# Kernel tuning notes

Hardware: AMD Instinct MI355X
Metric: run time of the kernel (lower is better)

The kernel has to match this reference:

```python
import jax, jax.numpy as jnp
import numpy as np

B, N, D = 8, 128, 256
EPS = 1e-5


def _layernorm(x, g, b):
    m = jnp.mean(x, axis=-1, keepdims=True)
    v = jnp.mean(jnp.square(x - m), axis=-1, keepdims=True)
    return (x - m) * jax.lax.rsqrt(v + EPS) * g + b


def setup_inputs() -> dict:
    key = jax.random.key(0)
    ks = jax.random.split(key, 24)
    s = 0.05  # param init scale
    return {
        "text": jax.random.normal(ks[0], (B, N, D), jnp.float32),
        "adj1": jax.random.uniform(ks[1], (B, N, N), jnp.float32),
        "adj2": jax.random.uniform(ks[2], (B, N, N), jnp.float32),
        "edge1": jax.random.normal(ks[3], (B, N, N, D), jnp.float32) * 0.1,
        "edge2": jax.random.normal(ks[4], (B, N, N, D), jnp.float32) * 0.1,
        "textmask": jnp.ones((B, N), jnp.float32),
        "weight": jax.random.normal(ks[5], (D, D), jnp.float32) * s,
        "bias": jax.random.normal(ks[6], (D,), jnp.float32) * s,
        "gamma": jnp.ones((D,), jnp.float32),
        "beta": jnp.zeros((D,), jnp.float32),
        "fuse1_w": jax.random.normal(ks[7], (2 * D, D), jnp.float32) * s,
        "fuse2_w": jax.random.normal(ks[8], (2 * D, D), jnp.float32) * s,
        "fc3_w": jax.random.normal(ks[9], (2 * D, D), jnp.float32) * s,
        "fc1_w0": jax.random.normal(ks[10], (3 * D, D), jnp.float32) * s,
        "fc1_w1": jax.random.normal(ks[11], (D, 1), jnp.float32) * s,
        "fc1_b1": jnp.zeros((1,), jnp.float32),
        "fc2_w0": jax.random.normal(ks[12], (3 * D, D), jnp.float32) * s,
        "fc2_w1": jax.random.normal(ks[13], (D, 1), jnp.float32) * s,
        "fc2_b1": jnp.zeros((1,), jnp.float32),
        "align_lin": jax.random.normal(ks[14], (D, D), jnp.float32) * s,
        "align_bias": jax.random.normal(ks[15], (D,), jnp.float32) * s,
    }


def reference(text, adj1, adj2, edge1, edge2, textmask, weight, bias, gamma,
              beta, fuse1_w, fuse2_w, fc3_w, fc1_w0, fc1_w1, fc1_b1,
              fc2_w0, fc2_w1, fc2_b1, align_lin, align_bias):
    d = text.shape[-1]
    # ---- SelfAlignment ----
    logits = jnp.einsum('bid,bjd->bij', text @ align_lin, text)
    mask_add = (1.0 - textmask)[:, None, :] * -1e20
    probs = jax.nn.softmax(logits + mask_add, axis=-1)
    outss = jnp.einsum('bij,bjd->bid', probs, text) * textmask[..., None] + align_bias

    # ---- GCN body ----
    out = jax.nn.relu(text @ weight)  # [B,N,D]

    # edge contributions are loop-invariant: precompute once
    # torch cat([x,e]) @ W  ==  x @ W[:d] + e @ W[d:]
    e1_fuse = jnp.einsum('bijd,de->bije', edge1, fuse1_w[d:])
    e2_fuse = jnp.einsum('bijd,de->bije', edge2, fuse2_w[d:])
    e1_fc = jnp.einsum('bijd,de->bije', edge1, fc1_w0[2 * d:])
    e2_fc = jnp.einsum('bijd,de->bije', edge2, fc2_w0[2 * d:])

    denom1 = jnp.sum(adj1, axis=2, keepdims=True) + 1.0  # [B,N,1]
    denom2 = jnp.sum(adj2, axis=2, keepdims=True) + 1.0

    for _ in range(3):  # K = 3
        # text1[b,i,j] = out[b,i]; text2[b,i,j] = out[b,j]
        t_i1 = (out @ fc1_w0[:d])[:, :, None, :]        # text1 part, fc1
        t_j1 = (out @ fc1_w0[d:2 * d])[:, None, :, :]   # text2 part, fc1
        t_i2 = (out @ fc2_w0[:d])[:, :, None, :]
        t_j2 = (out @ fc2_w0[d:2 * d])[:, None, :, :]

        teout = jax.nn.relu((out @ fuse1_w[:d])[:, None, :, :] + e1_fuse)  # [B,N,N,D]
        tein = jax.nn.relu((out @ fuse2_w[:d])[:, None, :, :] + e2_fuse)

        s1 = jax.nn.sigmoid(jax.nn.relu(t_i1 + t_j1 + e1_fc) @ fc1_w1 + fc1_b1)[..., 0]  # [B,N,N]
        s2 = jax.nn.sigmoid(jax.nn.relu(t_i2 + t_j2 + e2_fc) @ fc2_w1 + fc2_b1)[..., 0]

        out1 = jnp.einsum('bij,bijd->bid', adj1 * s1, teout) / denom1
        out2 = jnp.einsum('bij,bijd->bid', adj2 * s2, tein) / denom2

        out = jax.nn.relu(out1 @ fc3_w[:d] + out2 @ fc3_w[d:]) + out + bias
        out = _layernorm(out, gamma, beta)  # dropout = identity (eval)
    return out, outss
```

## Files before the change

### kernel.cpp

```cpp
#include <hip/hip_runtime.h>

typedef unsigned short u16;
typedef unsigned int u32;
typedef __attribute__((ext_vector_type(8))) short bf16x8;
typedef __attribute__((ext_vector_type(4))) float f32x4;

__device__ __forceinline__ u16 f2bf(float f) {
  u32 u = __float_as_uint(f);
  return (u16)((u + 0x7fffu + ((u >> 16) & 1u)) >> 16);
}

__device__ __forceinline__ void glds16(const void* g, void* l) {
  __builtin_amdgcn_global_load_lds(
      (const __attribute__((address_space(1))) unsigned int*)g,
      (__attribute__((address_space(3))) unsigned int*)l, 16, 0, 0);
}

__device__ __forceinline__ float4 unpack4(const u16* p) {
  uint2 a = *(const uint2*)p;
  float4 r;
  r.x = __uint_as_float(a.x << 16);
  r.y = __uint_as_float(a.x & 0xffff0000u);
  r.z = __uint_as_float(a.y << 16);
  r.w = __uint_as_float(a.y & 0xffff0000u);
  return r;
}

__global__ __launch_bounds__(256) void gemm_edge(
    const float* __restrict__ Af, const u16* __restrict__ Bt,
    u16* __restrict__ E) {
  __shared__ __align__(16) u16 Asm[8192];
  __shared__ __align__(16) u16 Bsm[8192];
  const int tid = threadIdx.x, lane = tid & 63, w = tid >> 6;
  const int m = lane & 15, q = lane >> 4;
  const int p = blockIdx.x;
  const int rt = (p & 7) * 128 + (p >> 5);
  const int ct = (p >> 3) & 3;
  const int wrow = (w & 1) * 64, wcol = (w >> 1) * 64;
  const float* Ab = Af + (long)rt * 32768;
  const char* Bb = (const char*)Bt + (long)ct * 65536;
  f32x4 acc[4][4];
#pragma unroll
  for (int r = 0; r < 4; ++r)
#pragma unroll
    for (int c = 0; c < 4; ++c) acc[r][c] = (f32x4){0.f, 0.f, 0.f, 0.f};

  for (int kc = 0; kc < 4; ++kc) {
#pragma unroll
    for (int it = 0; it < 8; ++it) {
      int f = it * 256 + tid;
      int r = f >> 4, c4 = (f & 15) * 4;
      float4 v = *(const float4*)(Ab + (long)r * 256 + kc * 64 + c4);
      ushort4 h;
      h.x = f2bf(v.x); h.y = f2bf(v.y); h.z = f2bf(v.z); h.w = f2bf(v.w);
      *(ushort4*)((char*)Asm + r * 128 + ((c4 * 2) ^ ((r & 7) * 16))) = h;
    }
#pragma unroll
    for (int t = 0; t < 4; ++t)
      glds16(Bb + kc * 16384 + t * 4096 + tid * 16,
             (char*)Bsm + t * 4096 + tid * 16);
    __syncthreads();
#pragma unroll
    for (int s = 0; s < 2; ++s) {
      const int ko2 = (s * 32 + q * 8) * 2;
      bf16x8 av[4], bv[4];
#pragma unroll
      for (int r = 0; r < 4; ++r) {
        int row = wrow + r * 16 + m;
        av[r] = *(const bf16x8*)((const char*)Asm + row * 128 +
                                 (ko2 ^ ((row & 7) * 16)));
      }
#pragma unroll
      for (int c = 0; c < 4; ++c) {
        int col = wcol + c * 16 + m;
        bv[c] = *(const bf16x8*)((const char*)Bsm + col * 128 +
                                 (ko2 ^ ((col & 7) * 16)));
      }
#pragma unroll
      for (int r = 0; r < 4; ++r)
#pragma unroll
        for (int c = 0; c < 4; ++c)
          acc[r][c] = __builtin_amdgcn_mfma_f32_16x16x32_bf16(
              av[r], bv[c], acc[r][c], 0, 0, 0);
    }
    __syncthreads();
  }
#pragma unroll
  for (int r = 0; r < 4; ++r)
#pragma unroll
    for (int c = 0; c < 4; ++c)
#pragma unroll
      for (int g = 0; g < 4; ++g) {
        long gr = (long)rt * 128 + wrow + r * 16 + q * 4 + g;
        int gc = ct * 128 + wcol + c * 16 + m;
        E[gr * 512 + gc] = f2bf(acc[r][c][g]);
      }
}

template<int K, int RF, bool OUT_BF16, bool RELU0, bool SUM2>
__global__ __launch_bounds__(256) void gemm_mfma(
    const float* __restrict__ A, const u16* __restrict__ Bt,
    void* __restrict__ Cv, int Ntot, float* __restrict__ relu_dst,
    const float* __restrict__ A2) {
  constexpr int ROWS = RF * 16;
  constexpr int LD = 72;
  __shared__ __align__(16) u16 Asm[ROWS * LD];
  __shared__ __align__(16) u16 Bsm[256 * LD];
  const int tid = threadIdx.x;
  const int lane = tid & 63;
  const int w = tid >> 6;
  const int m = lane & 15;
  const int q = lane >> 4;
  const int wcol = w * 64;
  const long rowbase = (long)blockIdx.x * ROWS;
  const long colbase = (long)blockIdx.y * 256;
  f32x4 acc[RF][4];
#pragma unroll
  for (int r = 0; r < RF; ++r)
#pragma unroll
    for (int c = 0; c < 4; ++c) acc[r][c] = (f32x4){0.f, 0.f, 0.f, 0.f};

  for (int kc = 0; kc < K / 64; ++kc) {
    const int kb = kc * 64;
#pragma unroll
    for (int it = 0; it < RF; ++it) {
      int f = it * 256 + tid;
      int r = f >> 4, c4 = (f & 15) * 4;
      float4 v = *(const float4*)(A + (rowbase + r) * K + kb + c4);
      if (SUM2) {
        float4 v2 = *(const float4*)(A2 + (rowbase + r) * K + kb + c4);
        v.x += v2.x; v.y += v2.y; v.z += v2.z; v.w += v2.w;
      }
      ushort4 h;
      h.x = f2bf(v.x); h.y = f2bf(v.y); h.z = f2bf(v.z); h.w = f2bf(v.w);
      *(ushort4*)&Asm[r * LD + c4] = h;
    }
#pragma unroll
    for (int it = 0; it < 8; ++it) {
      int f = it * 256 + tid;
      int c = f >> 3, k8 = (f & 7) * 8;
      *(uint4*)&Bsm[c * LD + k8] =
          *(const uint4*)(Bt + (colbase + c) * K + kb + k8);
    }
    __syncthreads();
#pragma unroll
    for (int s = 0; s < 2; ++s) {
      const int ko = s * 32 + q * 8;
      bf16x8 av[RF], bv[4];
#pragma unroll
      for (int r = 0; r < RF; ++r)
        av[r] = *(const bf16x8*)&Asm[(r * 16 + m) * LD + ko];
#pragma unroll
      for (int c = 0; c < 4; ++c)
        bv[c] = *(const bf16x8*)&Bsm[(wcol + c * 16 + m) * LD + ko];
#pragma unroll
      for (int r = 0; r < RF; ++r)
#pragma unroll
        for (int c = 0; c < 4; ++c)
          acc[r][c] = __builtin_amdgcn_mfma_f32_16x16x32_bf16(
              av[r], bv[c], acc[r][c], 0, 0, 0);
    }
    __syncthreads();
  }
#pragma unroll
  for (int r = 0; r < RF; ++r)
#pragma unroll
    for (int c = 0; c < 4; ++c)
#pragma unroll
      for (int g = 0; g < 4; ++g) {
        long gr = rowbase + r * 16 + q * 4 + g;
        long gc = colbase + wcol + c * 16 + m;
        float v = acc[r][c][g];
        if (OUT_BF16) ((u16*)Cv)[gr * Ntot + gc] = f2bf(v);
        else          ((float*)Cv)[gr * Ntot + gc] = v;
        if (RELU0) {
          if (gc < 256) relu_dst[gr * 256 + gc] = fmaxf(v, 0.f);
        }
      }
}

__global__ __launch_bounds__(256) void prep_bt(
    const float* __restrict__ weight, const float* __restrict__ align_lin,
    const float* __restrict__ fuse1_w, const float* __restrict__ fuse2_w,
    const float* __restrict__ fc1_w0, const float* __restrict__ fc2_w0,
    const float* __restrict__ fc3_w,
    u16* BtE1, u16* BtE2, u16* BtW0, u16* BtLoop, u16* BtFc3) {
  int g = blockIdx.x * 256 + threadIdx.x;
  if (g < 262144) {
    int t = g & 131071;
    int col = t >> 8, k = t & 255;
    float v;
    if (g < 131072)
      v = (col < 256) ? fuse1_w[(256 + k) * 256 + col]
                      : fc1_w0[(512 + k) * 256 + (col - 256)];
    else
      v = (col < 256) ? fuse2_w[(256 + k) * 256 + col]
                      : fc2_w0[(512 + k) * 256 + (col - 256)];
    int ct = col >> 7, cc = col & 127, kc = k >> 6, kk = k & 63;
    u16* dst = (g < 131072) ? BtE1 : BtE2;
    dst[ct * 32768 + kc * 8192 + cc * 64 + (kk ^ ((cc & 7) * 8))] = f2bf(v);
  } else if (g < 393216) {
    int t = g - 262144;
    int c = t >> 8, k = t & 255;
    float v = (c < 256) ? weight[k * 256 + c] : align_lin[k * 256 + (c - 256)];
    BtW0[t] = f2bf(v);
  } else if (g < 786432) {
    int t = g - 393216;
    int c = t >> 8, k = t & 255;
    int seg = c >> 8, cc = c & 255;
    float v;
    if      (seg == 0) v = fuse1_w[k * 256 + cc];
    else if (seg == 1) v = fuse2_w[k * 256 + cc];
    else if (seg == 2) v = fc1_w0[k * 256 + cc];
    else if (seg == 3) v = fc1_w0[(256 + k) * 256 + cc];
    else if (seg == 4) v = fc2_w0[k * 256 + cc];
    else               v = fc2_w0[(256 + k) * 256 + cc];
    BtLoop[t] = f2bf(v);
  } else {
    int t = g - 786432;
    int c = t >> 9, k = t & 511;
    BtFc3[t] = f2bf(fc3_w[k * 256 + c]);
  }
}

__global__ __launch_bounds__(128) void align_kernel(
    const float* __restrict__ text, const float* __restrict__ T0,
    const float* __restrict__ textmask, const float* __restrict__ align_bias,
    float* __restrict__ outss) {
  const int bi = blockIdx.x;
  const int b = bi >> 7;
  const int tid = threadIdx.x;
  __shared__ float ta[256];
  __shared__ float pr[128];
  __shared__ float red[128];
  ta[tid]       = T0[(long)bi * 512 + 256 + tid];
  ta[tid + 128] = T0[(long)bi * 512 + 384 + tid];
  __syncthreads();
  const float* trow = text + (long)(b * 128 + tid) * 256;
  float dot = 0.f;
  for (int d = 0; d < 256; d += 4) {
    float4 t4 = *(const float4*)(trow + d);
    dot += t4.x * ta[d] + t4.y * ta[d + 1] + t4.z * ta[d + 2] + t4.w * ta[d + 3];
  }
  float logit = dot + (1.0f - textmask[b * 128 + tid]) * -1e20f;
  pr[tid] = logit;
  red[tid] = logit;
  __syncthreads();
  for (int off = 64; off; off >>= 1) {
    if (tid < off) red[tid] = fmaxf(red[tid], red[tid + off]);
    __syncthreads();
  }
  float mx = red[0];
  __syncthreads();
  float e = __expf(pr[tid] - mx);
  red[tid] = e;
  __syncthreads();
  for (int off = 64; off; off >>= 1) {
    if (tid < off) red[tid] += red[tid + off];
    __syncthreads();
  }
  float inv = 1.0f / red[0];
  __syncthreads();
  pr[tid] = e * inv;
  __syncthreads();
  const float mi = textmask[bi];
  for (int h = 0; h < 2; ++h) {
    int d = tid + h * 128;
    float s = 0.f;
    for (int j = 0; j < 128; ++j)
      s += pr[j] * text[(long)(b * 128 + j) * 256 + d];
    outss[(long)bi * 256 + d] = s * mi + align_bias[d];
  }
}

__global__ __launch_bounds__(256) void fused_gate(
    const u16* __restrict__ E1, const u16* __restrict__ E2,
    const float* __restrict__ P, const float* __restrict__ adj1,
    const float* __restrict__ adj2, const float* __restrict__ fc1w1,
    const float* __restrict__ fc1b1, const float* __restrict__ fc2w1,
    const float* __restrict__ fc2b1, float* __restrict__ OUa,
    float* __restrict__ OUb) {
  const int tid = threadIdx.x, lane = tid & 63, w = tid >> 6;
  const int bi = blockIdx.x >> 1, half = blockIdx.x & 1;
  const int b = bi >> 7;
  const int d4 = lane * 4;
  const long rowi = (long)bi * 1536;
  const long ebase = (long)bi * 65536;
  const int abase = bi * 128;
  float* __restrict__ OU = half ? OUb : OUa;

  __shared__ float sA[64], sB[64];
  __shared__ float redA[4][256], redB[4][256];
  __shared__ float dInv[2];

  if (tid < 64) sA[tid] = adj1[abase + half * 64 + tid];
  else if (tid < 128) sB[tid - 64] = adj2[abase + half * 64 + (tid - 64)];
  if (w == 0) {
    float v = adj1[abase + lane] + adj1[abase + 64 + lane];
#pragma unroll
    for (int off = 32; off; off >>= 1) v += __shfl_xor(v, off);
    if (lane == 0) dInv[0] = 1.f / (1.f + v);
  } else if (w == 1) {
    float v = adj2[abase + lane] + adj2[abase + 64 + lane];
#pragma unroll
    for (int off = 32; off; off >>= 1) v += __shfl_xor(v, off);
    if (lane == 0) dInv[1] = 1.f / (1.f + v);
  }
  __syncthreads();

  const float4 ti1 = *(const float4*)(P + rowi + 512 + d4);
  const float4 ti2 = *(const float4*)(P + rowi + 1024 + d4);
  const float4 w1v = *(const float4*)(fc1w1 + d4);
  const float4 w2v = *(const float4*)(fc2w1 + d4);
  const float b1 = fc1b1[0], b2 = fc2b1[0];

  float4 acc1 = {0.f, 0.f, 0.f, 0.f}, acc2 = {0.f, 0.f, 0.f, 0.f};

#pragma unroll 2
  for (int t = 0; t < 16; ++t) {
    const int jl = w * 16 + t;
    const int j = half * 64 + jl;
    const long er = ebase + (long)j * 512;
    const long rowj = (long)((b << 7) + j) * 1536;
    float4 e1c = unpack4(E1 + er + 256 + d4);
    float4 e2c = unpack4(E2 + er + 256 + d4);
    float4 t1 = *(const float4*)(P + rowj + 768 + d4);
    float4 t2 = *(const float4*)(P + rowj + 1280 + d4);
    float z1 = fmaxf(ti1.x + t1.x + e1c.x, 0.f) * w1v.x +
               fmaxf(ti1.y + t1.y + e1c.y, 0.f) * w1v.y +
               fmaxf(ti1.z + t1.z + e1c.z, 0.f) * w1v.z +
               fmaxf(ti1.w + t1.w + e1c.w, 0.f) * w1v.w;
    float z2 = fmaxf(ti2.x + t2.x + e2c.x, 0.f) * w2v.x +
               fmaxf(ti2.y + t2.y + e2c.y, 0.f) * w2v.y +
               fmaxf(ti2.z + t2.z + e2c.z, 0.f) * w2v.z +
               fmaxf(ti2.w + t2.w + e2c.w, 0.f) * w2v.w;
#pragma unroll
    for (int off = 1; off < 64; off <<= 1) {
      z1 += __shfl_xor(z1, off);
      z2 += __shfl_xor(z2, off);
    }
    float s1 = sA[jl] * __builtin_amdgcn_rcpf(1.f + __expf(-(z1 + b1)));
    float s2 = sB[jl] * __builtin_amdgcn_rcpf(1.f + __expf(-(z2 + b2)));
    float4 e1f = unpack4(E1 + er + d4);
    float4 e2f = unpack4(E2 + er + d4);
    float4 o1 = *(const float4*)(P + rowj + d4);
    float4 o2 = *(const float4*)(P + rowj + 256 + d4);
    acc1.x += s1 * fmaxf(o1.x + e1f.x, 0.f);
    acc1.y += s1 * fmaxf(o1.y + e1f.y, 0.f);
    acc1.z += s1 * fmaxf(o1.z + e1f.z, 0.f);
    acc1.w += s1 * fmaxf(o1.w + e1f.w, 0.f);
    acc2.x += s2 * fmaxf(o2.x + e2f.x, 0.f);
    acc2.y += s2 * fmaxf(o2.y + e2f.y, 0.f);
    acc2.z += s2 * fmaxf(o2.z + e2f.z, 0.f);
    acc2.w += s2 * fmaxf(o2.w + e2f.w, 0.f);
  }

  *(float4*)&redA[w][d4] = acc1;
  *(float4*)&redB[w][d4] = acc2;
  __syncthreads();
  float r1 = redA[0][tid] + redA[1][tid] + redA[2][tid] + redA[3][tid];
  float r2 = redB[0][tid] + redB[1][tid] + redB[2][tid] + redB[3][tid];
  OU[(long)bi * 512 + tid] = r1 * dInv[0];
  OU[(long)bi * 512 + 256 + tid] = r2 * dInv[1];
}

__global__ __launch_bounds__(256) void ln_kernel(
    const float* __restrict__ Y, const float* __restrict__ prev,
    const float* __restrict__ bias, const float* __restrict__ gamma,
    const float* __restrict__ beta, float* __restrict__ dst) {
  const int row = blockIdx.x, tid = threadIdx.x, lane = tid & 63, w = tid >> 6;
  const long idx = (long)row * 256 + tid;
  float v = fmaxf(Y[idx], 0.f) + prev[idx] + bias[tid];
  float s = v;
#pragma unroll
  for (int off = 32; off; off >>= 1) s += __shfl_xor(s, off);
  __shared__ float wsA[4], wsB[4];
  if (lane == 0) wsA[w] = s;
  __syncthreads();
  float mean = (wsA[0] + wsA[1] + wsA[2] + wsA[3]) * (1.0f / 256.0f);
  float c = v - mean;
  float s2 = c * c;
#pragma unroll
  for (int off = 32; off; off >>= 1) s2 += __shfl_xor(s2, off);
  if (lane == 0) wsB[w] = s2;
  __syncthreads();
  float var = (wsB[0] + wsB[1] + wsB[2] + wsB[3]) * (1.0f / 256.0f);
  dst[idx] = c * rsqrtf(var + 1e-5f) * gamma[tid] + beta[tid];
}

extern "C" void kernel_launch(void* const* d_in, const int* in_sizes, int n_in,
                              void* d_out, int out_size, void* d_ws, size_t ws_size,
                              hipStream_t stream) {
  const float* text      = (const float*)d_in[0];
  const float* adj1      = (const float*)d_in[1];
  const float* adj2      = (const float*)d_in[2];
  const float* edge1     = (const float*)d_in[3];
  const float* edge2     = (const float*)d_in[4];
  const float* textmask  = (const float*)d_in[5];
  const float* weight    = (const float*)d_in[6];
  const float* bias      = (const float*)d_in[7];
  const float* gamma     = (const float*)d_in[8];
  const float* beta      = (const float*)d_in[9];
  const float* fuse1_w   = (const float*)d_in[10];
  const float* fuse2_w   = (const float*)d_in[11];
  const float* fc3_w     = (const float*)d_in[12];
  const float* fc1_w0    = (const float*)d_in[13];
  const float* fc1_w1    = (const float*)d_in[14];
  const float* fc1_b1    = (const float*)d_in[15];
  const float* fc2_w0    = (const float*)d_in[16];
  const float* fc2_w1    = (const float*)d_in[17];
  const float* fc2_b1    = (const float*)d_in[18];
  const float* align_lin = (const float*)d_in[19];
  const float* align_bias= (const float*)d_in[20];
  float* outF = (float*)d_out;

  char* w8 = (char*)d_ws;
  u16* E1   = (u16*)(w8 + 67108864);
  u16* E2   = (u16*)(w8 + 201326592);
  u16* BtE1 = (u16*)(w8 + 335544320);
  u16* BtE2 = BtE1 + 131072;
  u16* BtW0 = BtE2 + 131072;
  u16* BtLoop = BtW0 + 131072;
  u16* BtFc3  = BtLoop + 393216;
  float* P    = (float*)w8;
  float* T0   = P + 1572864;
  float* OUa  = T0 + 524288;
  float* OUb  = OUa + 524288;
  float* outb = OUb + 524288;
  float* Yb   = outb + 262144;

  prep_bt<<<3584, 256, 0, stream>>>(weight, align_lin, fuse1_w, fuse2_w,
                                    fc1_w0, fc2_w0, fc3_w,
                                    BtE1, BtE2, BtW0, BtLoop, BtFc3);
  gemm_edge<<<4096, 256, 0, stream>>>(edge1, BtE1, E1);
  gemm_edge<<<4096, 256, 0, stream>>>(edge2, BtE2, E2);
  gemm_mfma<256, 2, false, true, false><<<dim3(32, 2), 256, 0, stream>>>(
      text, BtW0, T0, 512, outb, nullptr);
  align_kernel<<<1024, 128, 0, stream>>>(text, T0, textmask, align_bias,
                                         outF + 262144);
  for (int it = 0; it < 3; ++it) {
    gemm_mfma<256, 2, false, false, false><<<dim3(32, 6), 256, 0, stream>>>(
        outb, BtLoop, P, 1536, nullptr, nullptr);
    fused_gate<<<2048, 256, 0, stream>>>(E1, E2, P, adj1, adj2, fc1_w1, fc1_b1,
                                         fc2_w1, fc2_b1, OUa, OUb);
    gemm_mfma<512, 2, false, false, true><<<dim3(32, 1), 256, 0, stream>>>(
        OUa, BtFc3, Yb, 256, nullptr, OUb);
    ln_kernel<<<1024, 256, 0, stream>>>(Yb, outb, bias, gamma, beta,
                                        (it == 2) ? outF : outb);
  }
}
```

Measured before the change: 739.7 us.

## Double-buffer A tiles with register prefetch, read B directly from global

Both GEMM kernels now prefetch the next K-chunk of the fp32 A operand into registers while the current chunk is converted and stored into a double-buffered LDS tile, with a single barrier per iteration instead of two. The B operand is no longer staged through LDS; each wave reads its bf16 fragments straight from global memory, relying on cache reuse. The small GEMMs also get a column-fragment template parameter and smaller tiles so more blocks are launched. This aims to hide global load latency and raise occupancy, at the cost of more register pressure and redundant global reads of B.

```diff
diff --git a/kernel.cpp b/kernel.cpp
--- a/kernel.cpp
+++ b/kernel.cpp
@@ -8,12 +8,6 @@
 __device__ __forceinline__ u16 f2bf(float f) {
   u32 u = __float_as_uint(f);
   return (u16)((u + 0x7fffu + ((u >> 16) & 1u)) >> 16);
-}
-
-__device__ __forceinline__ void glds16(const void* g, void* l) {
-  __builtin_amdgcn_global_load_lds(
-      (const __attribute__((address_space(1))) unsigned int*)g,
-      (__attribute__((address_space(3))) unsigned int*)l, 16, 0, 0);
 }
 
 __device__ __forceinline__ float4 unpack4(const u16* p) {
@@ -26,11 +20,16 @@
   return r;
 }
 
+__device__ __forceinline__ void barrier_lgkm() {
+  asm volatile("s_waitcnt lgkmcnt(0)" ::: "memory");
+  __builtin_amdgcn_s_barrier();
+  asm volatile("" ::: "memory");
+}
+
 __global__ __launch_bounds__(256) void gemm_edge(
     const float* __restrict__ Af, const u16* __restrict__ Bt,
     u16* __restrict__ E) {
-  __shared__ __align__(16) u16 Asm[8192];
-  __shared__ __align__(16) u16 Bsm[8192];
+  __shared__ __align__(16) u16 Asm[2][8192];
   const int tid = threadIdx.x, lane = tid & 63, w = tid >> 6;
   const int m = lane & 15, q = lane >> 4;
   const int p = blockIdx.x;
@@ -39,42 +38,50 @@
   const int wrow = (w & 1) * 64, wcol = (w >> 1) * 64;
   const float* Ab = Af + (long)rt * 32768;
   const char* Bb = (const char*)Bt + (long)ct * 65536;
+  const int r0 = tid >> 4, c4 = (tid & 15) * 4;
   f32x4 acc[4][4];
 #pragma unroll
   for (int r = 0; r < 4; ++r)
 #pragma unroll
     for (int c = 0; c < 4; ++c) acc[r][c] = (f32x4){0.f, 0.f, 0.f, 0.f};
 
+  float4 pre[8];
+#pragma unroll
+  for (int it = 0; it < 8; ++it)
+    pre[it] = *(const float4*)(Ab + (long)(it * 16 + r0) * 256 + c4);
+
+#pragma unroll
   for (int kc = 0; kc < 4; ++kc) {
+    char* As = (char*)Asm[kc & 1];
 #pragma unroll
     for (int it = 0; it < 8; ++it) {
-      int f = it * 256 + tid;
-      int r = f >> 4, c4 = (f & 15) * 4;
-      float4 v = *(const float4*)(Ab + (long)r * 256 + kc * 64 + c4);
+      int r = it * 16 + r0;
       ushort4 h;
-      h.x = f2bf(v.x); h.y = f2bf(v.y); h.z = f2bf(v.z); h.w = f2bf(v.w);
-      *(ushort4*)((char*)Asm + r * 128 + ((c4 * 2) ^ ((r & 7) * 16))) = h;
-    }
-#pragma unroll
-    for (int t = 0; t < 4; ++t)
-      glds16(Bb + kc * 16384 + t * 4096 + tid * 16,
-             (char*)Bsm + t * 4096 + tid * 16);
-    __syncthreads();
+      h.x = f2bf(pre[it].x); h.y = f2bf(pre[it].y);
+      h.z = f2bf(pre[it].z); h.w = f2bf(pre[it].w);
+      *(ushort4*)(As + r * 128 + ((c4 * 2) ^ ((r & 7) * 16))) = h;
+    }
+    if (kc < 3) {
+#pragma unroll
+      for (int it = 0; it < 8; ++it)
+        pre[it] = *(const float4*)(Ab + (long)(it * 16 + r0) * 256 +
+                                   (kc + 1) * 64 + c4);
+    }
+    barrier_lgkm();
 #pragma unroll
     for (int s = 0; s < 2; ++s) {
       const int ko2 = (s * 32 + q * 8) * 2;
       bf16x8 av[4], bv[4];
 #pragma unroll
+      for (int c = 0; c < 4; ++c) {
+        int col = wcol + c * 16 + m;
+        bv[c] = *(const bf16x8*)(Bb + kc * 16384 + col * 128 +
+                                 (ko2 ^ ((col & 7) * 16)));
+      }
+#pragma unroll
       for (int r = 0; r < 4; ++r) {
         int row = wrow + r * 16 + m;
-        av[r] = *(const bf16x8*)((const char*)Asm + row * 128 +
-                                 (ko2 ^ ((row & 7) * 16)));
-      }
-#pragma unroll
-      for (int c = 0; c < 4; ++c) {
-        int col = wcol + c * 16 + m;
-        bv[c] = *(const bf16x8*)((const char*)Bsm + col * 128 +
-                                 (ko2 ^ ((col & 7) * 16)));
+        av[r] = *(const bf16x8*)(As + row * 128 + (ko2 ^ ((row & 7) * 16)));
       }
 #pragma unroll
       for (int r = 0; r < 4; ++r)
@@ -83,7 +90,6 @@
           acc[r][c] = __builtin_amdgcn_mfma_f32_16x16x32_bf16(
               av[r], bv[c], acc[r][c], 0, 0, 0);
     }
-    __syncthreads();
   }
 #pragma unroll
   for (int r = 0; r < 4; ++r)
@@ -97,83 +103,93 @@
       }
 }
 
-template<int K, int RF, bool OUT_BF16, bool RELU0, bool SUM2>
+template<int K, int RF, int CF, bool OUT_BF16, bool RELU0, bool SUM2>
 __global__ __launch_bounds__(256) void gemm_mfma(
     const float* __restrict__ A, const u16* __restrict__ Bt,
     void* __restrict__ Cv, int Ntot, float* __restrict__ relu_dst,
     const float* __restrict__ A2) {
   constexpr int ROWS = RF * 16;
   constexpr int LD = 72;
-  __shared__ __align__(16) u16 Asm[ROWS * LD];
-  __shared__ __align__(16) u16 Bsm[256 * LD];
+  __shared__ __align__(16) u16 Asm[2][ROWS * LD];
   const int tid = threadIdx.x;
   const int lane = tid & 63;
   const int w = tid >> 6;
   const int m = lane & 15;
   const int q = lane >> 4;
-  const int wcol = w * 64;
+  const int wcol = w * (CF * 16);
   const long rowbase = (long)blockIdx.x * ROWS;
-  const long colbase = (long)blockIdx.y * 256;
-  f32x4 acc[RF][4];
+  const long colbase = (long)blockIdx.y * (CF * 64);
+  const int r0 = tid >> 4, c4 = (tid & 15) * 4;
+  f32x4 acc[RF][CF];
 #pragma unroll
   for (int r = 0; r < RF; ++r)
 #pragma unroll
-    for (int c = 0; c < 4; ++c) acc[r][c] = (f32x4){0.f, 0.f, 0.f, 0.f};
-
+    for (int c = 0; c < CF; ++c) acc[r][c] = (f32x4){0.f, 0.f, 0.f, 0.f};
+
+  float4 pre[RF], pre2[RF];
+#pragma unroll
+  for (int it = 0; it < RF; ++it) {
+    pre[it] = *(const float4*)(A + (rowbase + it * 16 + r0) * K + c4);
+    if constexpr (SUM2)
+      pre2[it] = *(const float4*)(A2 + (rowbase + it * 16 + r0) * K + c4);
+  }
+
+#pragma unroll
   for (int kc = 0; kc < K / 64; ++kc) {
-    const int kb = kc * 64;
+    u16* As = (u16*)Asm[kc & 1];
 #pragma unroll
     for (int it = 0; it < RF; ++it) {
-      int f = it * 256 + tid;
-      int r = f >> 4, c4 = (f & 15) * 4;
-      float4 v = *(const float4*)(A + (rowbase + r) * K + kb + c4);
-      if (SUM2) {
-        float4 v2 = *(const float4*)(A2 + (rowbase + r) * K + kb + c4);
-        v.x += v2.x; v.y += v2.y; v.z += v2.z; v.w += v2.w;
+      float4 v = pre[it];
+      if constexpr (SUM2) {
+        v.x += pre2[it].x; v.y += pre2[it].y;
+        v.z += pre2[it].z; v.w += pre2[it].w;
       }
       ushort4 h;
       h.x = f2bf(v.x); h.y = f2bf(v.y); h.z = f2bf(v.z); h.w = f2bf(v.w);
-      *(ushort4*)&Asm[r * LD + c4] = h;
-    }
-#pragma unroll
-    for (int it = 0; it < 8; ++it) {
-      int f = it * 256 + tid;
-      int c = f >> 3, k8 = (f & 7) * 8;
-      *(uint4*)&Bsm[c * LD + k8] =
-          *(const uint4*)(Bt + (colbase + c) * K + kb + k8);
-    }
-    __syncthreads();
+      *(ushort4*)&As[(it * 16 + r0) * LD + c4] = h;
+    }
+    if (kc + 1 < K / 64) {
+#pragma unroll
+      for (int it = 0; it < RF; ++it) {
+        pre[it] = *(const float4*)(A + (rowbase + it * 16 + r0) * K +
+                                   (kc + 1) * 64 + c4);
+        if constexpr (SUM2)
+          pre2[it] = *(const float4*)(A2 + (rowbase + it * 16 + r0) * K +
+                                      (kc + 1) * 64 + c4);
+      }
+    }
+    barrier_lgkm();
 #pragma unroll
     for (int s = 0; s < 2; ++s) {
       const int ko = s * 32 + q * 8;
-      bf16x8 av[RF], bv[4];
+      bf16x8 av[RF], bv[CF];
+#pragma unroll
+      for (int c = 0; c < CF; ++c)
+        bv[c] = *(const bf16x8*)(Bt + (long)(colbase + wcol + c * 16 + m) * K +
+                                 kc * 64 + ko);
 #pragma unroll
       for (int r = 0; r < RF; ++r)
-        av[r] = *(const bf16x8*)&Asm[(r * 16 + m) * LD + ko];
-#pragma unroll
-      for (int c = 0; c < 4; ++c)
-        bv[c] = *(const bf16x8*)&Bsm[(wcol + c * 16 + m) * LD + ko];
+        av[r] = *(const bf16x8*)&As[(r * 16 + m) * LD + ko];
 #pragma unroll
       for (int r = 0; r < RF; ++r)
 #pragma unroll
-        for (int c = 0; c < 4; ++c)
+        for (int c = 0; c < CF; ++c)
           acc[r][c] = __builtin_amdgcn_mfma_f32_16x16x32_bf16(
               av[r], bv[c], acc[r][c], 0, 0, 0);
     }
-    __syncthreads();
   }
 #pragma unroll
   for (int r = 0; r < RF; ++r)
 #pragma unroll
-    for (int c = 0; c < 4; ++c)
+    for (int c = 0; c < CF; ++c)
 #pragma unroll
       for (int g = 0; g < 4; ++g) {
         long gr = rowbase + r * 16 + q * 4 + g;
         long gc = colbase + wcol + c * 16 + m;
         float v = acc[r][c][g];
-        if (OUT_BF16) ((u16*)Cv)[gr * Ntot + gc] = f2bf(v);
-        else          ((float*)Cv)[gr * Ntot + gc] = v;
-        if (RELU0) {
+        if constexpr (OUT_BF16) ((u16*)Cv)[gr * Ntot + gc] = f2bf(v);
+        else                    ((float*)Cv)[gr * Ntot + gc] = v;
+        if constexpr (RELU0) {
           if (gc < 256) relu_dst[gr * 256 + gc] = fmaxf(v, 0.f);
         }
       }
@@ -434,16 +450,16 @@
                                     BtE1, BtE2, BtW0, BtLoop, BtFc3);
   gemm_edge<<<4096, 256, 0, stream>>>(edge1, BtE1, E1);
   gemm_edge<<<4096, 256, 0, stream>>>(edge2, BtE2, E2);
-  gemm_mfma<256, 2, false, true, false><<<dim3(32, 2), 256, 0, stream>>>(
+  gemm_mfma<256, 2, 2, false, true, false><<<dim3(32, 4), 256, 0, stream>>>(
       text, BtW0, T0, 512, outb, nullptr);
   align_kernel<<<1024, 128, 0, stream>>>(text, T0, textmask, align_bias,
                                          outF + 262144);
   for (int it = 0; it < 3; ++it) {
-    gemm_mfma<256, 2, false, false, false><<<dim3(32, 6), 256, 0, stream>>>(
+    gemm_mfma<256, 2, 2, false, false, false><<<dim3(32, 12), 256, 0, stream>>>(
         outb, BtLoop, P, 1536, nullptr, nullptr);
     fused_gate<<<2048, 256, 0, stream>>>(E1, E2, P, adj1, adj2, fc1_w1, fc1_b1,
                                          fc2_w1, fc2_b1, OUa, OUb);
-    gemm_mfma<512, 2, false, false, true><<<dim3(32, 1), 256, 0, stream>>>(
+    gemm_mfma<512, 1, 2, false, false, true><<<dim3(64, 2), 256, 0, stream>>>(
         OUa, BtFc3, Yb, 256, nullptr, OUb);
     ln_kernel<<<1024, 256, 0, stream>>>(Yb, outb, bias, gamma, beta,
                                         (it == 2) ? outF : outb);
```

Measured after the change: 737.9 us. No clear change (-0.2%).
